# Performance work log

Measured on AMD Instinct MI355X. Metric: run time of the kernel, lower is better.

The kernel has to match this reference:

```python
import jax, jax.numpy as jnp
import numpy as np
from jax import lax

DT = 0.025
CLIP = 1e11  # soft-clip scale used in the original: y + CLIP*tanh(st/CLIP)


def setup_inputs() -> dict:
    key = jax.random.key(0)
    ks = jax.random.split(key, 5)
    B, S, D, H = 8, 512, 64, 128
    X = jax.random.normal(ks[0], (B, S, D), dtype=jnp.float32)
    init_W = jax.random.normal(ks[1], (H, D), dtype=jnp.float32)
    init_b = jax.random.normal(ks[2], (H,), dtype=jnp.float32)
    # torch Linear layout: [out_features, in_features]
    vf_A_W = jax.random.normal(ks[3], (H * H, D + 1), dtype=jnp.float32) * (1.0 / H ** 0.5)
    vf_B_W = jax.random.normal(ks[4], (H, D + 1), dtype=jnp.float32)
    return {"X": X, "init_W": init_W, "init_b": init_b, "vf_A_W": vf_A_W, "vf_B_W": vf_B_W}


def reference(X, init_W, init_b, vf_A_W, vf_B_W):
    B, S, D = X.shape
    H = init_W.shape[0]
    # time channel (constant 1) prepended, scaled by dt
    inp = jnp.concatenate([jnp.ones((B, S, 1), X.dtype), X], axis=-1) * DT  # (B,S,D+1)
    y0 = X[:, 0] @ init_W.T + init_b                                        # (B,H)
    inp_t = inp[:, 1:]                                                      # (B,S-1,D+1)
    # A(x_t): (B,S-1,H,H); B(x_t): (B,S-1,H)
    As = jnp.einsum('bsd,od->bso', inp_t, vf_A_W).reshape(B, S - 1, H, H)
    Bs = jnp.einsum('bsd,hd->bsh', inp_t, vf_B_W)

    def step(y, AB):
        A, b = AB  # A: (B,H,H), b: (B,H)
        st = jnp.einsum('bij,bj->bi', A, y) + b
        y_new = y + CLIP * jnp.tanh(st / CLIP)
        return y_new, y_new

    _, ys = lax.scan(step, y0, (As.transpose(1, 0, 2, 3), Bs.transpose(1, 0, 2)))
    ys = jnp.concatenate([y0[:, None], ys.transpose(1, 0, 2)], axis=1)  # (B,S,H)
    return ys
```

## Files before the change

kernel.cpp:

```cpp
#include <hip/hip_runtime.h>
#include <hip/hip_bf16.h>

#define DT 0.025f
#define Bz 8
#define Sz 512
#define Dz 64
#define Hz 128
#define NT 511
#define OO (Hz * Hz)
#define KK (Dz + 1)
#define CHUNK 16

using short8 = __attribute__((ext_vector_type(8))) short;
using f32x4  = __attribute__((ext_vector_type(4))) float;
using u16x8  = __attribute__((ext_vector_type(8))) unsigned short;
using u16x4  = __attribute__((ext_vector_type(4))) unsigned short;

__device__ __forceinline__ float bf2f(unsigned short u) {
    union { unsigned int i; float f; } v;
    v.i = ((unsigned int)u) << 16;
    return v.f;
}
__device__ __forceinline__ unsigned short f2bf(float f) {
    union { float f; unsigned int i; } v;
    v.f = f;
    unsigned int u = v.i;
    return (unsigned short)((u + 0x7FFFu + ((u >> 16) & 1u)) >> 16);
}

__device__ __forceinline__ void dma16(const void* g, void* s) {
    __builtin_amdgcn_global_load_lds(
        (const __attribute__((address_space(1))) unsigned int*)g,
        (__attribute__((address_space(3))) unsigned int*)s, 16, 0, 0);
}

__global__ __launch_bounds__(256) void k_wsplit(const float* __restrict__ WA,
                                                unsigned short* __restrict__ Wh,
                                                unsigned short* __restrict__ Wl,
                                                float* __restrict__ WA0d) {
    int idx = blockIdx.x * 256 + threadIdx.x;
    int o = idx >> 3, u = idx & 7;
    const float* wr = WA + (size_t)o * KK + 1 + u * 8;
    u16x8 h = {}, lo = {};
#pragma unroll
    for (int j = 0; j < 8; ++j) {
        float v = wr[j];
        unsigned short hh = f2bf(v);
        h[j] = hh;
        lo[j] = f2bf(v - bf2f(hh));
    }
    *(u16x8*)(Wh + (size_t)o * 64 + u * 8) = h;
    *(u16x8*)(Wl + (size_t)o * 64 + u * 8) = lo;
    if (u == 0) WA0d[o] = DT * WA[(size_t)o * KK];
}

__global__ __launch_bounds__(256) void k_prep(const float* __restrict__ X,
                                              unsigned short* __restrict__ Xh,
                                              int t0, int Lsteps, int Lpad) {
    int idx = blockIdx.x * 256 + threadIdx.x;
    int m = idx >> 3, u = idx & 7;
    int b = m / Lpad, lt = m - b * Lpad;
    u16x8 h = {};
    if (lt < Lsteps) {
        const float* xr = X + ((size_t)b * Sz + t0 + lt + 1) * Dz + u * 8;
#pragma unroll
        for (int j = 0; j < 8; ++j) h[j] = f2bf(xr[j] * DT);
    }
    *(u16x8*)(Xh + (size_t)m * 64 + u * 8) = h;
}

__global__ __launch_bounds__(256) void k_y0(const float* __restrict__ X,
                                            const float* __restrict__ W,
                                            const float* __restrict__ bias,
                                            float* __restrict__ out) {
    int idx = blockIdx.x * 256 + threadIdx.x;
    int b = idx >> 7, h = idx & 127;
    const float* xr = X + (size_t)b * Sz * Dz;
    const float* wr = W + (size_t)h * Dz;
    float acc = bias[h];
    for (int d = 0; d < Dz; ++d) acc += xr[d] * wr[d];
    out[(size_t)b * Sz * Hz + h] = acc;
}

__global__ __launch_bounds__(256) void k_bs(const float* __restrict__ X,
                                            const float* __restrict__ WB,
                                            float* __restrict__ Bs) {
    int idx = blockIdx.x * 256 + threadIdx.x;
    int bt = idx >> 7, h = idx & 127;
    int b = bt / NT, t = bt - b * NT;
    const float* xr = X + ((size_t)b * Sz + t + 1) * Dz;
    const float* wr = WB + (size_t)h * KK;
    float acc = wr[0];
    for (int k = 0; k < Dz; ++k) acc += xr[k] * wr[1 + k];
    Bs[(size_t)bt * Hz + h] = acc * DT;
}

__global__ __launch_bounds__(256, 3) void k_gemm_mfma(
    const unsigned short* __restrict__ Xh,
    const unsigned short* __restrict__ Wh, const unsigned short* __restrict__ Wl,
    const float* __restrict__ WA0d, unsigned short* __restrict__ As) {
    const int tid = threadIdx.x;
    const int w = tid >> 6, l = tid & 63;
    const int lr = l & 15, lg = l >> 4;
    const int wbt = w >> 1, wo = w & 1;
    const int o0 = blockIdx.x * 128;
    const int bt0 = blockIdx.y * 128;

    __shared__ __align__(16) unsigned short L[3 * 8192];

#pragma unroll
    for (int q = 0; q < 4; ++q) {
        int seg = w * 4 + q;
        int du = seg * 64 + l;
        int row = du >> 3;
        int su = (du & ~7) | ((du & 7) ^ (row & 7));
        dma16(Xh + (size_t)bt0 * 64 + su * 8, &L[0 * 8192 + seg * 512]);
        dma16(Wh + (size_t)o0 * 64 + su * 8, &L[1 * 8192 + seg * 512]);
        dma16(Wl + (size_t)o0 * 64 + su * 8, &L[2 * 8192 + seg * 512]);
    }
    __syncthreads();

    f32x4 acc[4][4] = {};
    const unsigned short* Xh_l = &L[0];
    const unsigned short* Wh_l = &L[8192];
    const unsigned short* Wl_l = &L[16384];

#pragma unroll
    for (int kk = 0; kk < 2; ++kk) {
        short8 xh[4], wh[4], wl[4];
#pragma unroll
        for (int t = 0; t < 4; ++t) {
            int btr = wbt * 64 + t * 16 + lr;
            int orr = wo * 64 + t * 16 + lr;
            int ux = (kk * 4 + lg) ^ (btr & 7);
            int uw = (kk * 4 + lg) ^ (orr & 7);
            xh[t] = *(const short8*)&Xh_l[btr * 64 + ux * 8];
            wh[t] = *(const short8*)&Wh_l[orr * 64 + uw * 8];
            wl[t] = *(const short8*)&Wl_l[orr * 64 + uw * 8];
        }
#pragma unroll
        for (int ot = 0; ot < 4; ++ot)
#pragma unroll
            for (int bt = 0; bt < 4; ++bt) {
                acc[ot][bt] = __builtin_amdgcn_mfma_f32_16x16x32_bf16(
                    wh[ot], xh[bt], acc[ot][bt], 0, 0, 0);
                acc[ot][bt] = __builtin_amdgcn_mfma_f32_16x16x32_bf16(
                    wl[ot], xh[bt], acc[ot][bt], 0, 0, 0);
            }
    }

    __syncthreads();
    unsigned short* T = &L[0];
#pragma unroll
    for (int ot = 0; ot < 4; ++ot) {
        int obase = wo * 64 + ot * 16 + lg * 4;
        float4 wa = *(const float4*)&WA0d[o0 + obase];
#pragma unroll
        for (int bt = 0; bt < 4; ++bt) {
            int btl = wbt * 64 + bt * 16 + lr;
            u16x4 pk;
            pk[0] = f2bf(acc[ot][bt][0] + wa.x);
            pk[1] = f2bf(acc[ot][bt][1] + wa.y);
            pk[2] = f2bf(acc[ot][bt][2] + wa.z);
            pk[3] = f2bf(acc[ot][bt][3] + wa.w);
            int up = (obase >> 2) ^ ((btl & 15) << 1);
            *(u16x4*)&T[btl * 128 + up * 4] = pk;
        }
    }
    __syncthreads();
    const int lane16 = tid & 15;
    const int segb = tid >> 4;
    const int chunkg0 = bt0 >> 4;
#pragma unroll
    for (int it = 0; it < 8; ++it) {
        int seg = it * 16 + segb;
        int k = seg & 15;
        size_t chunkg = (size_t)chunkg0 + (seg >> 4);
        int up = (lane16 * 2) ^ (k << 1);
        u16x8 val = *(const u16x8*)&T[seg * 128 + up * 4];
        *(u16x8*)(As + (chunkg * 16 + k) * (size_t)OO + o0 + lane16 * 8) = val;
    }
}

__device__ __forceinline__ void stage_a(const unsigned short* Astep,
                                        unsigned short* AbufF, int buf,
                                        int w, int l) {
#pragma unroll
    for (int q = 0; q < 2; ++q) {
        int seg = w * 2 + q;
        int du = seg * 64 + l;
        int row = du >> 4, cu = du & 15;
        int su = (du & ~15) | (cu ^ (row & 7));
        dma16(Astep + (size_t)su * 8, &AbufF[buf * OO + seg * 512]);
    }
}

__global__ __launch_bounds__(1024) void k_chunk_a(
    const unsigned short* __restrict__ As, const float* __restrict__ Bs,
    float* __restrict__ Dm, float* __restrict__ Vv,
    int t0, int Lsteps, int NCs) {
    const int cs = blockIdx.x, b = blockIdx.y;
    const int tid = threadIdx.x;
    const int w = tid >> 6, l = tid & 63;
    const int lr = l & 15, lg = l >> 4;
    const int wr = w >> 2, wc = w & 3;
    int Lc = Lsteps - cs * CHUNK; if (Lc > CHUNK) Lc = CHUNK;

    __shared__ __align__(16) unsigned short AbufF[3 * OO];
    __shared__ __align__(16) unsigned short Pt[129 * Hz];
    __shared__ __align__(16) float BsL[CHUNK][Hz];

    for (int idx = tid; idx < 129 * Hz; idx += 1024) {
        int row = idx >> 7, col = idx & 127;
        unsigned short val = (row < Hz && row == col) ? (unsigned short)0x3F80
                                                      : (unsigned short)0;
        int unit = (col >> 3) ^ (row & 7);
        Pt[(row << 7) | (unit << 3) | (col & 7)] = val;
    }
    const int t0c = t0 + cs * CHUNK;
    for (int idx = tid; idx < Lc * Hz; idx += 1024) {
        int row = idx >> 7, col = idx & 127;
        BsL[row][col] = Bs[((size_t)b * NT + t0c + row) * Hz + col];
    }

    const unsigned short* AsC = As + (size_t)(b * NCs + cs) * 16 * OO;

    float idv[2][2][4];
#pragma unroll
    for (int tix = 0; tix < 2; ++tix)
#pragma unroll
        for (int tjx = 0; tjx < 2; ++tjx) {
            int i0 = 32 * wr + 16 * tix + 4 * lg;
            int j = 32 * wc + 16 * tjx + lr;
#pragma unroll
            for (int r = 0; r < 4; ++r)
                idv[tix][tjx][r] = (i0 + r == j) ? 1.f : 0.f;
        }

    stage_a(AsC, AbufF, 0, w, l);
    if (Lc > 1) stage_a(AsC + OO, AbufF, 1, w, l);

    f32x4 acc[2][2] = {};
    f32x4 vacc = {};
    int b0 = 0, b1 = 1, b2 = 2;
    const int kxor = lr & 7;

    for (int k = 0; k < Lc; ++k) {
        if (k + 1 < Lc) {
            asm volatile("s_waitcnt vmcnt(2) lgkmcnt(0)" ::: "memory");
        } else {
            asm volatile("s_waitcnt vmcnt(0) lgkmcnt(0)" ::: "memory");
        }
        __builtin_amdgcn_s_barrier();
        asm volatile("" ::: "memory");

        if (k + 2 < Lc) stage_a(AsC + (size_t)(k + 2) * OO, AbufF, b2, w, l);

        const unsigned short* Ac = &AbufF[b0 * OO];
#pragma unroll
        for (int kt = 0; kt < 4; ++kt) {
            const int uoff = ((kt * 4 + lg) ^ kxor) << 3;
            short8 af0 = *(const short8*)&Ac[((32 * wr + lr) << 7) | uoff];
            short8 af1 = *(const short8*)&Ac[((32 * wr + 16 + lr) << 7) | uoff];
            short8 bf0 = *(const short8*)&Pt[((32 * wc + lr) << 7) | uoff];
            short8 bf1 = *(const short8*)&Pt[((32 * wc + 16 + lr) << 7) | uoff];
            acc[0][0] = __builtin_amdgcn_mfma_f32_16x16x32_bf16(af0, bf0,
                                                                acc[0][0], 0, 0, 0);
            acc[0][1] = __builtin_amdgcn_mfma_f32_16x16x32_bf16(af0, bf1,
                                                                acc[0][1], 0, 0, 0);
            acc[1][0] = __builtin_amdgcn_mfma_f32_16x16x32_bf16(af1, bf0,
                                                                acc[1][0], 0, 0, 0);
            acc[1][1] = __builtin_amdgcn_mfma_f32_16x16x32_bf16(af1, bf1,
                                                                acc[1][1], 0, 0, 0);
            if (w < 8) {
                short8 afv = *(const short8*)&Ac[((16 * w + lr) << 7) | uoff];
                short8 vf = *(const short8*)&Pt[(128 << 7) | ((kt * 4 + lg) << 3)];
                vacc = __builtin_amdgcn_mfma_f32_16x16x32_bf16(afv, vf, vacc,
                                                               0, 0, 0);
            }
        }

        asm volatile("s_waitcnt lgkmcnt(0)" ::: "memory");
        __builtin_amdgcn_s_barrier();
        asm volatile("" ::: "memory");

#pragma unroll
        for (int tix = 0; tix < 2; ++tix)
#pragma unroll
            for (int tjx = 0; tjx < 2; ++tjx) {
                int i0 = 32 * wr + 16 * tix + 4 * lg;
                int j = 32 * wc + 16 * tjx + lr;
                u16x4 pk;
#pragma unroll
                for (int r = 0; r < 4; ++r)
                    pk[r] = f2bf(acc[tix][tjx][r] + idv[tix][tjx][r]);
                int unit = (i0 >> 3) ^ (j & 7);
                *(u16x4*)&Pt[(j << 7) | (unit << 3) | (i0 & 7)] = pk;
            }
        if (w < 8 && lr == 0) {
            int i0 = 16 * w + 4 * lg;
            const float* bp = &BsL[k][i0];
            u16x4 pk;
#pragma unroll
            for (int r = 0; r < 4; ++r) {
                vacc[r] += bp[r];
                pk[r] = f2bf(vacc[r]);
            }
            *(u16x4*)&Pt[(128 << 7) | ((i0 >> 3) << 3) | (i0 & 7)] = pk;
        }
        int tmp = b0; b0 = b1; b1 = b2; b2 = tmp;
    }

    const size_t ci = (size_t)b * NCs + cs;
    float* D = Dm + ci * OO;
#pragma unroll
    for (int tix = 0; tix < 2; ++tix)
#pragma unroll
        for (int tjx = 0; tjx < 2; ++tjx) {
            int i0 = 32 * wr + 16 * tix + 4 * lg;
            int j = 32 * wc + 16 * tjx + lr;
#pragma unroll
            for (int r = 0; r < 4; ++r)
                D[(size_t)(i0 + r) * Hz + j] = acc[tix][tjx][r];
        }
    if (w < 8 && lr == 0) {
        int i0 = 16 * w + 4 * lg;
        float* V = Vv + ci * Hz;
#pragma unroll
        for (int r = 0; r < 4; ++r) V[i0 + r] = vacc[r];
    }
}

__global__ __launch_bounds__(1024) void k_chunk_b(
    const float* __restrict__ Dm, const float* __restrict__ Vv,
    float* __restrict__ out, int t0, int Lsteps, int NCs) {
    const int b = blockIdx.x, tid = threadIdx.x;
    const int i = tid >> 3, q = tid & 7;
    __shared__ __align__(16) float yv[2][Hz];
    __shared__ float VvL[32 * Hz];

    if (tid < Hz) yv[0][tid] = out[((size_t)b * Sz + t0) * Hz + tid];
    for (int idx = tid; idx < NCs * Hz; idx += 1024)
        VvL[idx] = Vv[(size_t)b * NCs * Hz + idx];
    __syncthreads();

    const float4* D0 = (const float4*)(Dm + (size_t)b * NCs * OO);
    const int off = i * 32 + q * 4;
    float4 cur[4], n1[4], n2[4];
#pragma unroll
    for (int v = 0; v < 4; ++v) cur[v] = D0[off + v];
    {
        int c1i = (NCs > 1) ? 1 : 0;
        const float4* Dn = D0 + (size_t)c1i * (OO / 4);
#pragma unroll
        for (int v = 0; v < 4; ++v) n1[v] = Dn[off + v];
    }

    for (int cs = 0; cs < NCs; ++cs) {
        int nc2 = (cs + 2 < NCs) ? cs + 2 : NCs - 1;
        const float4* Dn = D0 + (size_t)nc2 * (OO / 4);
#pragma unroll
        for (int v = 0; v < 4; ++v) n2[v] = Dn[off + v];

        const int cb = cs & 1;
        const float* yp = &yv[cb][q * 16];
        float s = 0.f;
#pragma unroll
        for (int v = 0; v < 4; ++v)
            s += cur[v].x * yp[v * 4 + 0] + cur[v].y * yp[v * 4 + 1] +
                 cur[v].z * yp[v * 4 + 2] + cur[v].w * yp[v * 4 + 3];
        s += __shfl_xor(s, 1);
        s += __shfl_xor(s, 2);
        s += __shfl_xor(s, 4);

        if (q == 0) {
            float yn = yv[cb][i] + s + VvL[cs * Hz + i];
            yv[cb ^ 1][i] = yn;
            int t_end = t0 + (cs + 1) * CHUNK;
            if (t_end < Sz)
                out[((size_t)b * Sz + t_end) * Hz + i] = yn;
        }
        asm volatile("s_waitcnt lgkmcnt(0)" ::: "memory");
        __builtin_amdgcn_s_barrier();
        asm volatile("" ::: "memory");
#pragma unroll
        for (int v = 0; v < 4; ++v) { cur[v] = n1[v]; n1[v] = n2[v]; }
    }
}

__global__ __launch_bounds__(1024) void k_chunk_c(
    const unsigned short* __restrict__ As, const float* __restrict__ Bs,
    float* __restrict__ out, int t0, int Lsteps, int NCs) {
    const int cs = blockIdx.x, b = blockIdx.y;
    const int tid = threadIdx.x;
    const int i = tid >> 3, p = tid & 7;
    const int t0c = t0 + cs * CHUNK;
    int Lc = Lsteps - cs * CHUNK; if (Lc > CHUNK) Lc = CHUNK;
    __shared__ __align__(16) float y[2][Hz];

    if (tid < Hz) y[0][tid] = out[((size_t)b * Sz + t0c) * Hz + tid];
    __syncthreads();

    const unsigned short* Abp = As + (size_t)(b * NCs + cs) * 16 * OO +
                                i * Hz + p * 16;
    const float* Bsb = Bs + (size_t)b * NT * Hz;
    float* outb = out + (size_t)b * Sz * Hz;

    u16x8 c0 = *(const u16x8*)(Abp);
    u16x8 c1 = *(const u16x8*)(Abp + 8);
    int l1 = (Lc > 1) ? 1 : 0;
    u16x8 d0 = *(const u16x8*)(Abp + (size_t)l1 * OO);
    u16x8 d1 = *(const u16x8*)(Abp + (size_t)l1 * OO + 8);

    for (int lt = 0; lt < Lc; ++lt) {
        int ln = lt + 2; if (ln > Lc - 1) ln = Lc - 1;
        u16x8 e0 = *(const u16x8*)(Abp + (size_t)ln * OO);
        u16x8 e1 = *(const u16x8*)(Abp + (size_t)ln * OO + 8);

        const int cur = lt & 1;
        const float4* yp = (const float4*)&y[cur][p * 16];
        float4 y0v = yp[0], y1v = yp[1], y2v = yp[2], y3v = yp[3];

        float s;
        s  = bf2f(c0[0]) * y0v.x + bf2f(c0[1]) * y0v.y +
             bf2f(c0[2]) * y0v.z + bf2f(c0[3]) * y0v.w;
        s += bf2f(c0[4]) * y1v.x + bf2f(c0[5]) * y1v.y +
             bf2f(c0[6]) * y1v.z + bf2f(c0[7]) * y1v.w;
        s += bf2f(c1[0]) * y2v.x + bf2f(c1[1]) * y2v.y +
             bf2f(c1[2]) * y2v.z + bf2f(c1[3]) * y2v.w;
        s += bf2f(c1[4]) * y3v.x + bf2f(c1[5]) * y3v.y +
             bf2f(c1[6]) * y3v.z + bf2f(c1[7]) * y3v.w;
        s += __shfl_xor(s, 1);
        s += __shfl_xor(s, 2);
        s += __shfl_xor(s, 4);

        if (p == 0) {
            int t = t0c + lt;
            float st = s + Bsb[(size_t)t * Hz + i];
            float yn = y[cur][i] + st;
            y[cur ^ 1][i] = yn;
            if (((t + 1) & (CHUNK - 1)) != 0)
                outb[(size_t)(t + 1) * Hz + i] = yn;
        }
        c0 = d0; c1 = d1; d0 = e0; d1 = e1;
        asm volatile("s_waitcnt lgkmcnt(0)" ::: "memory");
        __builtin_amdgcn_s_barrier();
        asm volatile("" ::: "memory");
    }
}

__global__ __launch_bounds__(1024) void k_fused(const float* __restrict__ X,
                                                const float* __restrict__ initW,
                                                const float* __restrict__ initb,
                                                const float* __restrict__ WA,
                                                const float* __restrict__ WB,
                                                float* __restrict__ out) {
    const int b = blockIdx.x, tid = threadIdx.x;
    const int i = tid >> 3, p = tid & 7;
    __shared__ float y[2][Hz];
    __shared__ float u[KK];

    if (tid < Hz) {
        float a = initb[tid];
        const float* xr = X + (size_t)b * Sz * Dz;
        const float* wr = initW + (size_t)tid * Dz;
        for (int d = 0; d < Dz; ++d) a += xr[d] * wr[d];
        y[0][tid] = a;
        out[(size_t)b * Sz * Hz + tid] = a;
    }
    __syncthreads();

    for (int t = 0; t < NT; ++t) {
        if (tid < KK)
            u[tid] = (tid == 0) ? DT
                                : X[((size_t)b * Sz + t + 1) * Dz + tid - 1] * DT;
        __syncthreads();
        const int cur = t & 1;
        float partial = 0.f;
        for (int jj = 0; jj < 16; ++jj) {
            int j = p * 16 + jj;
            const float* wr = WA + (size_t)(i * Hz + j) * KK;
            float a = 0.f;
            for (int d = 0; d < KK; ++d) a += wr[d] * u[d];
            partial += a * y[cur][j];
        }
        partial += __shfl_xor(partial, 1);
        partial += __shfl_xor(partial, 2);
        partial += __shfl_xor(partial, 4);
        if (p == 0) {
            const float* wb = WB + (size_t)i * KK;
            float bv = 0.f;
            for (int d = 0; d < KK; ++d) bv += wb[d] * u[d];
            float yn = y[cur][i] + partial + bv;
            y[cur ^ 1][i] = yn;
            out[(size_t)b * Sz * Hz + (size_t)(t + 1) * Hz + i] = yn;
        }
        __syncthreads();
    }
}

extern "C" void kernel_launch(void* const* d_in, const int* in_sizes, int n_in,
                              void* d_out, int out_size, void* d_ws,
                              size_t ws_size, hipStream_t stream) {
    const float* X = (const float*)d_in[0];
    const float* initW = (const float*)d_in[1];
    const float* initb = (const float*)d_in[2];
    const float* WA = (const float*)d_in[3];
    const float* WB = (const float*)d_in[4];
    float* out = (float*)d_out;

    const size_t WH_OFF = 0;
    const size_t WL_OFF = 2097152;
    const size_t WA0_OFF = 4194304;
    const size_t XH_OFF = 4259840;
    const size_t BS_OFF = 5308416;
    const size_t base = 7401472;
    const size_t PER_SC = (size_t)Bz * OO * 4 +
                          (size_t)Bz * Hz * 4 +
                          (size_t)Bz * CHUNK * OO * 2;
    const int NC = (NT + CHUNK - 1) / CHUNK;

    long SC_max = (ws_size > base) ? (long)((ws_size - base) / PER_SC) : 0;
    if (SC_max >= 1) {
        if (SC_max > NC) SC_max = NC;
        int nS = (NC + (int)SC_max - 1) / (int)SC_max;
        int SC = (NC + nS - 1) / nS;

        unsigned short* Wh = (unsigned short*)((char*)d_ws + WH_OFF);
        unsigned short* Wl = (unsigned short*)((char*)d_ws + WL_OFF);
        float* WA0d = (float*)((char*)d_ws + WA0_OFF);
        unsigned short* Xh = (unsigned short*)((char*)d_ws + XH_OFF);
        float* Bs = (float*)((char*)d_ws + BS_OFF);
        float* Dm = (float*)((char*)d_ws + base);
        float* Vv = (float*)((char*)d_ws + base + (size_t)SC * Bz * OO * 4);
        unsigned short* As = (unsigned short*)((char*)d_ws + base +
                                               (size_t)SC * Bz * OO * 4 +
                                               (size_t)SC * Bz * Hz * 4);

        k_wsplit<<<512, 256, 0, stream>>>(WA, Wh, Wl, WA0d);
        k_y0<<<4, 256, 0, stream>>>(X, initW, initb, out);
        k_bs<<<2044, 256, 0, stream>>>(X, WB, Bs);

        for (int c0 = 0; c0 < NC; c0 += SC) {
            int t0 = c0 * CHUNK;
            int Lsteps = NT - t0;
            if (Lsteps > SC * CHUNK) Lsteps = SC * CHUNK;
            int NCs = (Lsteps + CHUNK - 1) / CHUNK;
            int Lpad = NCs * CHUNK;
            k_prep<<<4 * NCs, 256, 0, stream>>>(X, Xh, t0, Lsteps, Lpad);
            k_gemm_mfma<<<dim3(128, NCs), 256, 0, stream>>>(Xh, Wh, Wl, WA0d,
                                                            As);
            k_chunk_a<<<dim3(NCs, Bz), 1024, 0, stream>>>(As, Bs, Dm, Vv, t0,
                                                          Lsteps, NCs);
            k_chunk_b<<<Bz, 1024, 0, stream>>>(Dm, Vv, out, t0, Lsteps, NCs);
            k_chunk_c<<<dim3(NCs, Bz), 1024, 0, stream>>>(As, Bs, out, t0,
                                                          Lsteps, NCs);
        }
    } else {
        k_fused<<<Bz, 1024, 0, stream>>>(X, initW, initb, WA, WB, out);
    }
}
```

Baseline: 170.1 us.

## Load A chunk matrices straight to registers and double-buffer the product matrix

The chunk kernel stops staging each step's A matrix through a triple-buffered LDS ring with async DMA. Each wave now loads its A fragments directly from global memory into registers, prefetching one step ahead with two register sets. The running product Pt is ping-ponged between two LDS buffers, which removes one barrier per step. The bias-vector MFMA moves to the wc==0 waves, which reuse the A fragments they already hold, and the bf16 packing uses the hardware v_cvt_pk_bf16_f32 instruction. The cost is higher register pressure, and global-load latency now sits directly on the sequential step path.

```diff
diff --git a/kernel.cpp b/kernel.cpp
--- a/kernel.cpp
+++ b/kernel.cpp
@@ -26,6 +26,11 @@
     v.f = f;
     unsigned int u = v.i;
     return (unsigned short)((u + 0x7FFFu + ((u >> 16) & 1u)) >> 16);
+}
+__device__ __forceinline__ unsigned int cvt_pk_bf16(float lo, float hi) {
+    unsigned int r;
+    asm("v_cvt_pk_bf16_f32 %0, %1, %2" : "=v"(r) : "v"(lo), "v"(hi));
+    return r;
 }
 
 __device__ __forceinline__ void dma16(const void* g, void* s) {
@@ -182,19 +187,6 @@
     }
 }
 
-__device__ __forceinline__ void stage_a(const unsigned short* Astep,
-                                        unsigned short* AbufF, int buf,
-                                        int w, int l) {
-#pragma unroll
-    for (int q = 0; q < 2; ++q) {
-        int seg = w * 2 + q;
-        int du = seg * 64 + l;
-        int row = du >> 4, cu = du & 15;
-        int su = (du & ~15) | (cu ^ (row & 7));
-        dma16(Astep + (size_t)su * 8, &AbufF[buf * OO + seg * 512]);
-    }
-}
-
 __global__ __launch_bounds__(1024) void k_chunk_a(
     const unsigned short* __restrict__ As, const float* __restrict__ Bs,
     float* __restrict__ Dm, float* __restrict__ Vv,
@@ -206,8 +198,8 @@
     const int wr = w >> 2, wc = w & 3;
     int Lc = Lsteps - cs * CHUNK; if (Lc > CHUNK) Lc = CHUNK;
 
-    __shared__ __align__(16) unsigned short AbufF[3 * OO];
-    __shared__ __align__(16) unsigned short Pt[129 * Hz];
+    __shared__ __align__(16) unsigned short PtA[129 * Hz];
+    __shared__ __align__(16) unsigned short PtB[129 * Hz];
     __shared__ __align__(16) float BsL[CHUNK][Hz];
 
     for (int idx = tid; idx < 129 * Hz; idx += 1024) {
@@ -215,7 +207,7 @@
         unsigned short val = (row < Hz && row == col) ? (unsigned short)0x3F80
                                                       : (unsigned short)0;
         int unit = (col >> 3) ^ (row & 7);
-        Pt[(row << 7) | (unit << 3) | (col & 7)] = val;
+        PtA[(row << 7) | (unit << 3) | (col & 7)] = val;
     }
     const int t0c = t0 + cs * CHUNK;
     for (int idx = tid; idx < Lc * Hz; idx += 1024) {
@@ -225,7 +217,98 @@
 
     const unsigned short* AsC = As + (size_t)(b * NCs + cs) * 16 * OO;
 
-    float idv[2][2][4];
+    int rd[2][2];
+#pragma unroll
+    for (int tix = 0; tix < 2; ++tix)
+#pragma unroll
+        for (int tjx = 0; tjx < 2; ++tjx)
+            rd[tix][tjx] = (32 * wc + 16 * tjx + lr) -
+                           (32 * wr + 16 * tix + 4 * lg);
+
+    f32x4 acc[2][2] = {};
+    f32x4 vacc[2] = {};
+    short8 RA[4][2], RB[4][2];
+
+    auto loadA = [&](int k, short8(&R)[4][2]) {
+        const unsigned short* base = AsC + (size_t)k * OO;
+#pragma unroll
+        for (int kt = 0; kt < 4; ++kt)
+#pragma unroll
+            for (int tix = 0; tix < 2; ++tix)
+                R[kt][tix] = *(const short8*)(base +
+                    (32 * wr + 16 * tix + lr) * Hz + kt * 32 + lg * 8);
+    };
+
+    const unsigned short* ptc = PtA;
+    unsigned short* ptn = PtB;
+    const int kxor = lr & 7;
+
+    auto step = [&](int k, short8(&R)[4][2]) {
+#pragma unroll
+        for (int kt = 0; kt < 4; ++kt) {
+            const int uoff = ((kt * 4 + lg) ^ kxor) << 3;
+            short8 bf0 = *(const short8*)&ptc[((32 * wc + lr) << 7) | uoff];
+            short8 bf1 = *(const short8*)&ptc[((32 * wc + 16 + lr) << 7) | uoff];
+            short8 vf = *(const short8*)&ptc[(128 << 7) | ((kt * 4 + lg) << 3)];
+#pragma unroll
+            for (int tix = 0; tix < 2; ++tix) {
+                acc[tix][0] = __builtin_amdgcn_mfma_f32_16x16x32_bf16(
+                    R[kt][tix], bf0, acc[tix][0], 0, 0, 0);
+                acc[tix][1] = __builtin_amdgcn_mfma_f32_16x16x32_bf16(
+                    R[kt][tix], bf1, acc[tix][1], 0, 0, 0);
+                if (wc == 0)
+                    vacc[tix] = __builtin_amdgcn_mfma_f32_16x16x32_bf16(
+                        R[kt][tix], vf, vacc[tix], 0, 0, 0);
+            }
+        }
+#pragma unroll
+        for (int tix = 0; tix < 2; ++tix)
+#pragma unroll
+            for (int tjx = 0; tjx < 2; ++tjx) {
+                int i0 = 32 * wr + 16 * tix + 4 * lg;
+                int j = 32 * wc + 16 * tjx + lr;
+                float v0 = acc[tix][tjx][0] + ((0 == rd[tix][tjx]) ? 1.f : 0.f);
+                float v1 = acc[tix][tjx][1] + ((1 == rd[tix][tjx]) ? 1.f : 0.f);
+                float v2 = acc[tix][tjx][2] + ((2 == rd[tix][tjx]) ? 1.f : 0.f);
+                float v3 = acc[tix][tjx][3] + ((3 == rd[tix][tjx]) ? 1.f : 0.f);
+                uint2 pk;
+                pk.x = cvt_pk_bf16(v0, v1);
+                pk.y = cvt_pk_bf16(v2, v3);
+                int unit = (i0 >> 3) ^ (j & 7);
+                *(uint2*)&ptn[(j << 7) | (unit << 3) | (i0 & 7)] = pk;
+            }
+        if (wc == 0 && lr == 0) {
+#pragma unroll
+            for (int tix = 0; tix < 2; ++tix) {
+                int i0 = 32 * wr + 16 * tix + 4 * lg;
+                const float* bp = &BsL[k][i0];
+#pragma unroll
+                for (int r = 0; r < 4; ++r) vacc[tix][r] += bp[r];
+                uint2 pk;
+                pk.x = cvt_pk_bf16(vacc[tix][0], vacc[tix][1]);
+                pk.y = cvt_pk_bf16(vacc[tix][2], vacc[tix][3]);
+                *(uint2*)&ptn[(128 << 7) | i0] = pk;
+            }
+        }
+        asm volatile("s_waitcnt lgkmcnt(0)" ::: "memory");
+        __builtin_amdgcn_s_barrier();
+        asm volatile("" ::: "memory");
+        const unsigned short* t = ptc; ptc = ptn; ptn = (unsigned short*)t;
+    };
+
+    __syncthreads();
+    loadA(0, RA);
+    for (int k = 0; k < Lc; k += 2) {
+        if (k + 1 < Lc) loadA(k + 1, RB);
+        step(k, RA);
+        if (k + 1 < Lc) {
+            if (k + 2 < Lc) loadA(k + 2, RA);
+            step(k + 1, RB);
+        }
+    }
+
+    const size_t ci = (size_t)b * NCs + cs;
+    float* D = Dm + ci * OO;
 #pragma unroll
     for (int tix = 0; tix < 2; ++tix)
 #pragma unroll
@@ -234,100 +317,16 @@
             int j = 32 * wc + 16 * tjx + lr;
 #pragma unroll
             for (int r = 0; r < 4; ++r)
-                idv[tix][tjx][r] = (i0 + r == j) ? 1.f : 0.f;
-        }
-
-    stage_a(AsC, AbufF, 0, w, l);
-    if (Lc > 1) stage_a(AsC + OO, AbufF, 1, w, l);
-
-    f32x4 acc[2][2] = {};
-    f32x4 vacc = {};
-    int b0 = 0, b1 = 1, b2 = 2;
-    const int kxor = lr & 7;
-
-    for (int k = 0; k < Lc; ++k) {
-        if (k + 1 < Lc) {
-            asm volatile("s_waitcnt vmcnt(2) lgkmcnt(0)" ::: "memory");
-        } else {
-            asm volatile("s_waitcnt vmcnt(0) lgkmcnt(0)" ::: "memory");
-        }
-        __builtin_amdgcn_s_barrier();
-        asm volatile("" ::: "memory");
-
-        if (k + 2 < Lc) stage_a(AsC + (size_t)(k + 2) * OO, AbufF, b2, w, l);
-
-        const unsigned short* Ac = &AbufF[b0 * OO];
-#pragma unroll
-        for (int kt = 0; kt < 4; ++kt) {
-            const int uoff = ((kt * 4 + lg) ^ kxor) << 3;
-            short8 af0 = *(const short8*)&Ac[((32 * wr + lr) << 7) | uoff];
-            short8 af1 = *(const short8*)&Ac[((32 * wr + 16 + lr) << 7) | uoff];
-            short8 bf0 = *(const short8*)&Pt[((32 * wc + lr) << 7) | uoff];
-            short8 bf1 = *(const short8*)&Pt[((32 * wc + 16 + lr) << 7) | uoff];
-            acc[0][0] = __builtin_amdgcn_mfma_f32_16x16x32_bf16(af0, bf0,
-                                                                acc[0][0], 0, 0, 0);
-            acc[0][1] = __builtin_amdgcn_mfma_f32_16x16x32_bf16(af0, bf1,
-                                                                acc[0][1], 0, 0, 0);
-            acc[1][0] = __builtin_amdgcn_mfma_f32_16x16x32_bf16(af1, bf0,
-                                                                acc[1][0], 0, 0, 0);
-            acc[1][1] = __builtin_amdgcn_mfma_f32_16x16x32_bf16(af1, bf1,
-                                                                acc[1][1], 0, 0, 0);
-            if (w < 8) {
-                short8 afv = *(const short8*)&Ac[((16 * w + lr) << 7) | uoff];
-                short8 vf = *(const short8*)&Pt[(128 << 7) | ((kt * 4 + lg) << 3)];
-                vacc = __builtin_amdgcn_mfma_f32_16x16x32_bf16(afv, vf, vacc,
-                                                               0, 0, 0);
-            }
-        }
-
-        asm volatile("s_waitcnt lgkmcnt(0)" ::: "memory");
-        __builtin_amdgcn_s_barrier();
-        asm volatile("" ::: "memory");
-
-#pragma unroll
-        for (int tix = 0; tix < 2; ++tix)
-#pragma unroll
-            for (int tjx = 0; tjx < 2; ++tjx) {
-                int i0 = 32 * wr + 16 * tix + 4 * lg;
-                int j = 32 * wc + 16 * tjx + lr;
-                u16x4 pk;
-#pragma unroll
-                for (int r = 0; r < 4; ++r)
-                    pk[r] = f2bf(acc[tix][tjx][r] + idv[tix][tjx][r]);
-                int unit = (i0 >> 3) ^ (j & 7);
-                *(u16x4*)&Pt[(j << 7) | (unit << 3) | (i0 & 7)] = pk;
-            }
-        if (w < 8 && lr == 0) {
-            int i0 = 16 * w + 4 * lg;
-            const float* bp = &BsL[k][i0];
-            u16x4 pk;
-#pragma unroll
-            for (int r = 0; r < 4; ++r) {
-                vacc[r] += bp[r];
-                pk[r] = f2bf(vacc[r]);
-            }
-            *(u16x4*)&Pt[(128 << 7) | ((i0 >> 3) << 3) | (i0 & 7)] = pk;
-        }
-        int tmp = b0; b0 = b1; b1 = b2; b2 = tmp;
-    }
-
-    const size_t ci = (size_t)b * NCs + cs;
-    float* D = Dm + ci * OO;
-#pragma unroll
-    for (int tix = 0; tix < 2; ++tix)
-#pragma unroll
-        for (int tjx = 0; tjx < 2; ++tjx) {
+                D[(size_t)(i0 + r) * Hz + j] = acc[tix][tjx][r];
+        }
+    if (wc == 0 && lr == 0) {
+        float* V = Vv + ci * Hz;
+#pragma unroll
+        for (int tix = 0; tix < 2; ++tix) {
             int i0 = 32 * wr + 16 * tix + 4 * lg;
-            int j = 32 * wc + 16 * tjx + lr;
-#pragma unroll
-            for (int r = 0; r < 4; ++r)
-                D[(size_t)(i0 + r) * Hz + j] = acc[tix][tjx][r];
-        }
-    if (w < 8 && lr == 0) {
-        int i0 = 16 * w + 4 * lg;
-        float* V = Vv + ci * Hz;
-#pragma unroll
-        for (int r = 0; r < 4; ++r) V[i0 + r] = vacc[r];
+#pragma unroll
+            for (int r = 0; r < 4; ++r) V[i0 + r] = vacc[tix][r];
+        }
     }
 }
 
```

Result: slower. 226.5 us (+33.1%).

## Split chunk product kernel across two column halves to double block count

Applied to the files above, without the earlier changes.

The chunk-composition kernel now launches a third grid dimension of two, and each block computes only 64 of the 128 columns of the running transition-matrix product. Per-wave MFMA work and the Pt shared buffer are halved. The intent is to fill more CUs, since NCs*8 blocks may underfill the GPU. In exchange, each A tile is staged twice (once per half), which doubles global and LDS traffic for A, and only the first half computes the vector term.

```diff
diff --git a/kernel.cpp b/kernel.cpp
--- a/kernel.cpp
+++ b/kernel.cpp
@@ -199,21 +199,22 @@
     const unsigned short* __restrict__ As, const float* __restrict__ Bs,
     float* __restrict__ Dm, float* __restrict__ Vv,
     int t0, int Lsteps, int NCs) {
-    const int cs = blockIdx.x, b = blockIdx.y;
+    const int cs = blockIdx.x, b = blockIdx.y, ch = blockIdx.z;
     const int tid = threadIdx.x;
     const int w = tid >> 6, l = tid & 63;
     const int lr = l & 15, lg = l >> 4;
     const int wr = w >> 2, wc = w & 3;
+    const int jb = ch * 64;
     int Lc = Lsteps - cs * CHUNK; if (Lc > CHUNK) Lc = CHUNK;
 
     __shared__ __align__(16) unsigned short AbufF[3 * OO];
-    __shared__ __align__(16) unsigned short Pt[129 * Hz];
+    __shared__ __align__(16) unsigned short Pt[65 * Hz];
     __shared__ __align__(16) float BsL[CHUNK][Hz];
 
-    for (int idx = tid; idx < 129 * Hz; idx += 1024) {
+    for (int idx = tid; idx < 65 * Hz; idx += 1024) {
         int row = idx >> 7, col = idx & 127;
-        unsigned short val = (row < Hz && row == col) ? (unsigned short)0x3F80
-                                                      : (unsigned short)0;
+        unsigned short val = (row < 64 && col == jb + row)
+                                 ? (unsigned short)0x3F80 : (unsigned short)0;
         int unit = (col >> 3) ^ (row & 7);
         Pt[(row << 7) | (unit << 3) | (col & 7)] = val;
     }
@@ -225,22 +226,15 @@
 
     const unsigned short* AsC = As + (size_t)(b * NCs + cs) * 16 * OO;
 
-    float idv[2][2][4];
+    int rd[2];
 #pragma unroll
     for (int tix = 0; tix < 2; ++tix)
-#pragma unroll
-        for (int tjx = 0; tjx < 2; ++tjx) {
-            int i0 = 32 * wr + 16 * tix + 4 * lg;
-            int j = 32 * wc + 16 * tjx + lr;
-#pragma unroll
-            for (int r = 0; r < 4; ++r)
-                idv[tix][tjx][r] = (i0 + r == j) ? 1.f : 0.f;
-        }
+        rd[tix] = (jb + 16 * wc + lr) - (32 * wr + 16 * tix + 4 * lg);
 
     stage_a(AsC, AbufF, 0, w, l);
     if (Lc > 1) stage_a(AsC + OO, AbufF, 1, w, l);
 
-    f32x4 acc[2][2] = {};
+    f32x4 acc[2] = {};
     f32x4 vacc = {};
     int b0 = 0, b1 = 1, b2 = 2;
     const int kxor = lr & 7;
@@ -262,19 +256,14 @@
             const int uoff = ((kt * 4 + lg) ^ kxor) << 3;
             short8 af0 = *(const short8*)&Ac[((32 * wr + lr) << 7) | uoff];
             short8 af1 = *(const short8*)&Ac[((32 * wr + 16 + lr) << 7) | uoff];
-            short8 bf0 = *(const short8*)&Pt[((32 * wc + lr) << 7) | uoff];
-            short8 bf1 = *(const short8*)&Pt[((32 * wc + 16 + lr) << 7) | uoff];
-            acc[0][0] = __builtin_amdgcn_mfma_f32_16x16x32_bf16(af0, bf0,
-                                                                acc[0][0], 0, 0, 0);
-            acc[0][1] = __builtin_amdgcn_mfma_f32_16x16x32_bf16(af0, bf1,
-                                                                acc[0][1], 0, 0, 0);
-            acc[1][0] = __builtin_amdgcn_mfma_f32_16x16x32_bf16(af1, bf0,
-                                                                acc[1][0], 0, 0, 0);
-            acc[1][1] = __builtin_amdgcn_mfma_f32_16x16x32_bf16(af1, bf1,
-                                                                acc[1][1], 0, 0, 0);
-            if (w < 8) {
+            short8 bf  = *(const short8*)&Pt[((16 * wc + lr) << 7) | uoff];
+            acc[0] = __builtin_amdgcn_mfma_f32_16x16x32_bf16(af0, bf,
+                                                             acc[0], 0, 0, 0);
+            acc[1] = __builtin_amdgcn_mfma_f32_16x16x32_bf16(af1, bf,
+                                                             acc[1], 0, 0, 0);
+            if (w < 8 && ch == 0) {
                 short8 afv = *(const short8*)&Ac[((16 * w + lr) << 7) | uoff];
-                short8 vf = *(const short8*)&Pt[(128 << 7) | ((kt * 4 + lg) << 3)];
+                short8 vf = *(const short8*)&Pt[(64 << 7) | ((kt * 4 + lg) << 3)];
                 vacc = __builtin_amdgcn_mfma_f32_16x16x32_bf16(afv, vf, vacc,
                                                                0, 0, 0);
             }
@@ -285,19 +274,17 @@
         asm volatile("" ::: "memory");
 
 #pragma unroll
-        for (int tix = 0; tix < 2; ++tix)
-#pragma unroll
-            for (int tjx = 0; tjx < 2; ++tjx) {
-                int i0 = 32 * wr + 16 * tix + 4 * lg;
-                int j = 32 * wc + 16 * tjx + lr;
-                u16x4 pk;
-#pragma unroll
-                for (int r = 0; r < 4; ++r)
-                    pk[r] = f2bf(acc[tix][tjx][r] + idv[tix][tjx][r]);
-                int unit = (i0 >> 3) ^ (j & 7);
-                *(u16x4*)&Pt[(j << 7) | (unit << 3) | (i0 & 7)] = pk;
-            }
-        if (w < 8 && lr == 0) {
+        for (int tix = 0; tix < 2; ++tix) {
+            int i0 = 32 * wr + 16 * tix + 4 * lg;
+            int jl = 16 * wc + lr;
+            u16x4 pk;
+#pragma unroll
+            for (int r = 0; r < 4; ++r)
+                pk[r] = f2bf(acc[tix][r] + ((rd[tix] == r) ? 1.f : 0.f));
+            int unit = (i0 >> 3) ^ (jl & 7);
+            *(u16x4*)&Pt[(jl << 7) | (unit << 3) | (i0 & 7)] = pk;
+        }
+        if (w < 8 && ch == 0 && lr == 0) {
             int i0 = 16 * w + 4 * lg;
             const float* bp = &BsL[k][i0];
             u16x4 pk;
@@ -306,7 +293,7 @@
                 vacc[r] += bp[r];
                 pk[r] = f2bf(vacc[r]);
             }
-            *(u16x4*)&Pt[(128 << 7) | ((i0 >> 3) << 3) | (i0 & 7)] = pk;
+            *(u16x4*)&Pt[(64 << 7) | i0] = pk;
         }
         int tmp = b0; b0 = b1; b1 = b2; b2 = tmp;
     }
@@ -314,16 +301,14 @@
     const size_t ci = (size_t)b * NCs + cs;
     float* D = Dm + ci * OO;
 #pragma unroll
-    for (int tix = 0; tix < 2; ++tix)
-#pragma unroll
-        for (int tjx = 0; tjx < 2; ++tjx) {
-            int i0 = 32 * wr + 16 * tix + 4 * lg;
-            int j = 32 * wc + 16 * tjx + lr;
-#pragma unroll
-            for (int r = 0; r < 4; ++r)
-                D[(size_t)(i0 + r) * Hz + j] = acc[tix][tjx][r];
-        }
-    if (w < 8 && lr == 0) {
+    for (int tix = 0; tix < 2; ++tix) {
+        int i0 = 32 * wr + 16 * tix + 4 * lg;
+        int j = jb + 16 * wc + lr;
+#pragma unroll
+        for (int r = 0; r < 4; ++r)
+            D[(size_t)(i0 + r) * Hz + j] = acc[tix][r];
+    }
+    if (w < 8 && ch == 0 && lr == 0) {
         int i0 = 16 * w + 4 * lg;
         float* V = Vv + ci * Hz;
 #pragma unroll
@@ -550,8 +535,8 @@
             k_prep<<<4 * NCs, 256, 0, stream>>>(X, Xh, t0, Lsteps, Lpad);
             k_gemm_mfma<<<dim3(128, NCs), 256, 0, stream>>>(Xh, Wh, Wl, WA0d,
                                                             As);
-            k_chunk_a<<<dim3(NCs, Bz), 1024, 0, stream>>>(As, Bs, Dm, Vv, t0,
-                                                          Lsteps, NCs);
+            k_chunk_a<<<dim3(NCs, Bz, 2), 1024, 0, stream>>>(As, Bs, Dm, Vv,
+                                                             t0, Lsteps, NCs);
             k_chunk_b<<<Bz, 1024, 0, stream>>>(Dm, Vv, out, t0, Lsteps, NCs);
             k_chunk_c<<<dim3(NCs, Bz), 1024, 0, stream>>>(As, Bs, out, t0,
                                                           Lsteps, NCs);
```

Measured after the change: 189.4 us. 11.3% more time.
